# Kernel tuning notes

Hardware: AMD Instinct MI355X
Metric: run time of the kernel (lower is better)

Reference implementation:

```python
import jax, jax.numpy as jnp
import numpy as np

MD = 40                 # max_displacement
K = 2 * MD + 1          # 81 kernel size -> K*K = 6561 displacements


def setup_inputs() -> dict:
    key = jax.random.key(0)
    k1, k2 = jax.random.split(key)
    b, c, h, w = 2, 128, 64, 96
    x1 = jax.random.normal(k1, (b, c, h, w), dtype=jnp.float32)
    x2 = jax.random.normal(k2, (b, c, h, w), dtype=jnp.float32)
    return {"x1": x1, "x2": x2}


def reference(x1, x2):
    b, c, h, w = x1.shape
    # zero-pad x2 by MD on each spatial side (matches F.pad(x2, (pad,)*4))
    x2p = jnp.pad(x2, ((0, 0), (0, 0), (MD, MD), (MD, MD)))

    # Fused sliding-window correlation: scan over the K*K displacements,
    # slicing a (b,c,h,w) window of x2p and reducing over channels.
    # Avoids the (b,c,K^2,h,w) unfold blow-up entirely.
    def step(carry, s):
        dy = s // K
        dx = s % K
        win = jax.lax.dynamic_slice(x2p, (0, 0, dy, dx), (b, c, h, w))
        return carry, jnp.einsum('bchw,bchw->bhw', x1, win)

    _, corr = jax.lax.scan(step, None, jnp.arange(K * K))  # (K*K, b, h, w)
    corr = jnp.transpose(corr, (1, 0, 2, 3))               # (b, K*K, h, w)
    return corr / jnp.sqrt(jnp.float32(c))
```

## Files before the change

kernel.cpp:

```cpp
#include <hip/hip_runtime.h>

#define CH    128
#define HH    64
#define WW    96
#define MD    40
#define KD    81
#define HW    (HH*WW)
#define CHW   (CH*HW)
#define SCALE 0.08838834764831845f
#define LSTR  64
#define CHUNK (WW*LSTR)
#define WS2_USH ((size_t)2*HH*2*CHUNK)
#define NWG   (HH*KD*2)

typedef __attribute__((ext_vector_type(8))) short bf16x8;
typedef __attribute__((ext_vector_type(4))) float f32x4;

__device__ inline unsigned int pack2bf(float lo, float hi) {
    unsigned int a = __float_as_uint(lo), b = __float_as_uint(hi);
    a = (a + 0x7FFFu + ((a >> 16) & 1u)) >> 16;
    b = (b + 0x7FFFu + ((b >> 16) & 1u)) >> 16;
    return a | (b << 16);
}

__global__ __launch_bounds__(256) void prepack(
    const float* __restrict__ x1, const float* __restrict__ x2,
    unsigned short* __restrict__ ws)
{
    const int y = blockIdx.x;
    const int h = blockIdx.y & 1;
    const int t = blockIdx.y >> 1;
    const int b = blockIdx.z;

    const float* src = (t ? x2 : x1)
        + (size_t)b * CHW + (size_t)(h * 64) * HW + (size_t)y * WW;
    unsigned short* dst = ws + (size_t)t * WS2_USH
        + ((size_t)(b * HH + y) * 2 + h) * CHUNK;

    for (int j = threadIdx.x; j < 8 * WW; j += 256) {
        const int cg = j / WW;
        const int x  = j - cg * WW;
        const float* p = src + (size_t)(cg * 8) * HW + x;
        float f[8];
        #pragma unroll
        for (int i = 0; i < 8; ++i) f[i] = p[(size_t)i * HW];
        uint4 w;
        w.x = pack2bf(f[0], f[1]); w.y = pack2bf(f[2], f[3]);
        w.z = pack2bf(f[4], f[5]); w.w = pack2bf(f[6], f[7]);
        *reinterpret_cast<uint4*>(&dst[(size_t)x * LSTR + cg * 8]) = w;
    }
}

__global__ __launch_bounds__(256, 4) void corr_kernel(
    const unsigned short* __restrict__ ws, float* __restrict__ out)
{
    const int wg  = blockIdx.x;
    const int b   = (wg >= HH * KD) ? 1 : 0;
    const int rem = wg - b * (HH * KD);
    const int dy  = rem >> 6;
    const int y   = rem & 63;
    const int tid = threadIdx.x;

    float* outbase = out + ((size_t)b * (KD * KD) + (size_t)dy * KD) * HW
                         + (size_t)y * WW;

    const int y2 = y + dy - MD;
    if (y2 < 0 || y2 >= HH) {
        const float4 z = make_float4(0.f, 0.f, 0.f, 0.f);
        #pragma unroll
        for (int it = 0; it < 8; ++it) {
            const int idx = it * 256 + tid;
            if (idx < KD * (WW / 4)) {
                const int dx = idx / 24;
                const int x4 = idx - dx * 24;
                *reinterpret_cast<float4*>(outbase + (size_t)dx * HW + x4 * 4) = z;
            }
        }
        return;
    }

    __shared__ __align__(16) char smem[KD * WW * 4];
    float* sG = reinterpret_cast<float*>(smem);

    const unsigned short* wsA = ws + ((size_t)(b * HH + y ) * 2) * CHUNK;
    const unsigned short* wsB = ws + WS2_USH + ((size_t)(b * HH + y2) * 2) * CHUNK;

    const int lane = tid & 63;
    const int wave = tid >> 6;
    const int m0   = (wave >> 1) * 48;
    const int n0   = (wave & 1) * 48;
    const int lr   = lane & 15;
    const int q    = lane >> 4;

    f32x4 acc[3][3];
    #pragma unroll
    for (int i = 0; i < 3; ++i)
        #pragma unroll
        for (int j = 0; j < 3; ++j)
            acc[i][j] = (f32x4){0.f, 0.f, 0.f, 0.f};

    #pragma unroll
    for (int h = 0; h < 2; ++h) {
        const unsigned short* pA = wsA + (size_t)h * CHUNK;
        const unsigned short* pB = wsB + (size_t)h * CHUNK;
        #pragma unroll
        for (int kk = 0; kk < 2; ++kk) {
            const int cl = kk * 32 + q * 8;
            bf16x8 af[3], bg[3];
            #pragma unroll
            for (int i = 0; i < 3; ++i)
                af[i] = *reinterpret_cast<const bf16x8*>(&pB[(m0 + 16 * i + lr) * LSTR + cl]);
            #pragma unroll
            for (int j = 0; j < 3; ++j)
                bg[j] = *reinterpret_cast<const bf16x8*>(&pA[(n0 + 16 * j + lr) * LSTR + cl]);
            #pragma unroll
            for (int i = 0; i < 3; ++i)
                #pragma unroll
                for (int j = 0; j < 3; ++j)
                    acc[i][j] = __builtin_amdgcn_mfma_f32_16x16x32_bf16(
                        af[i], bg[j], acc[i][j], 0, 0, 0);
        }
    }

    #pragma unroll
    for (int i = 0; i < 3; ++i) {
        #pragma unroll
        for (int j = 0; j < 3; ++j) {
            const int col  = n0 + 16 * j + lr;
            const int rowb = m0 + 16 * i + q * 4;
            #pragma unroll
            for (int r = 0; r < 4; ++r) {
                const int dxv = (rowb + r) - col + MD;
                if ((unsigned)dxv < (unsigned)KD) {
                    const int w = (dxv * WW + col) ^ (((dxv >> 2) & 1) << 4);
                    sG[w] = acc[i][j][r] * SCALE;
                }
            }
        }
    }
    __syncthreads();

    int dx = tid / 24;
    int x  = 4 * tid - dx * WW;
    #pragma unroll
    for (int it = 0; it < 8; ++it) {
        if (it < 7 || tid < 152) {
            const int baddr = ((dx * WW + x) << 2) ^ (((dx >> 2) & 1) << 6);
            float4 v = *reinterpret_cast<const float4*>(smem + baddr);
            const int x2b = x + dx - MD;
            v.x = ((unsigned)(x2b + 0) < (unsigned)WW) ? v.x : 0.f;
            v.y = ((unsigned)(x2b + 1) < (unsigned)WW) ? v.y : 0.f;
            v.z = ((unsigned)(x2b + 2) < (unsigned)WW) ? v.z : 0.f;
            v.w = ((unsigned)(x2b + 3) < (unsigned)WW) ? v.w : 0.f;
            *reinterpret_cast<float4*>(outbase + (size_t)(dx * HW + x)) = v;
        }
        x += 64; dx += 10;
        if (x >= WW) { x -= WW; ++dx; }
    }
}

extern "C" void kernel_launch(void* const* d_in, const int* in_sizes, int n_in,
                              void* d_out, int out_size, void* d_ws, size_t ws_size,
                              hipStream_t stream) {
    const float* x1 = (const float*)d_in[0];
    const float* x2 = (const float*)d_in[1];
    float* out = (float*)d_out;
    unsigned short* ws = (unsigned short*)d_ws;

    hipLaunchKernelGGL(prepack, dim3(HH, 4, 2), dim3(256), 0, stream, x1, x2, ws);

    hipLaunchKernelGGL(corr_kernel, dim3(NWG), dim3(256), 0, stream, ws, out);
}
```

Before: 374.8 us.

## Make correlation workgroups persistent over dy to reuse x1 fragments in registers

```diff
diff --git a/kernel.cpp b/kernel.cpp
--- a/kernel.cpp
+++ b/kernel.cpp
@@ -8,10 +8,11 @@
 #define HW    (HH*WW)
 #define CHW   (CH*HW)
 #define SCALE 0.08838834764831845f
-#define LSTR  64
+#define LSTR  72
 #define CHUNK (WW*LSTR)
 #define WS2_USH ((size_t)2*HH*2*CHUNK)
-#define NWG   (HH*KD*2)
+#define NCH   16
+#define NWG   (2*HH*NCH)
 
 typedef __attribute__((ext_vector_type(8))) short bf16x8;
 typedef __attribute__((ext_vector_type(4))) float f32x4;
@@ -21,6 +22,12 @@
     a = (a + 0x7FFFu + ((a >> 16) & 1u)) >> 16;
     b = (b + 0x7FFFu + ((b >> 16) & 1u)) >> 16;
     return a | (b << 16);
+}
+
+__device__ __forceinline__ void gload16(const void* g, void* l) {
+    __builtin_amdgcn_global_load_lds(
+        (const __attribute__((address_space(1))) void*)g,
+        (__attribute__((address_space(3))) void*)l, 16, 0, 0);
 }
 
 __global__ __launch_bounds__(256) void prepack(
@@ -55,35 +62,14 @@
     const unsigned short* __restrict__ ws, float* __restrict__ out)
 {
     const int wg  = blockIdx.x;
-    const int b   = (wg >= HH * KD) ? 1 : 0;
-    const int rem = wg - b * (HH * KD);
-    const int dy  = rem >> 6;
-    const int y   = rem & 63;
+    const int y   = wg & 63;
+    const int c   = (wg >> 6) & 15;
+    const int b   = wg >> 10;
     const int tid = threadIdx.x;
 
-    float* outbase = out + ((size_t)b * (KD * KD) + (size_t)dy * KD) * HW
-                         + (size_t)y * WW;
-
-    const int y2 = y + dy - MD;
-    if (y2 < 0 || y2 >= HH) {
-        const float4 z = make_float4(0.f, 0.f, 0.f, 0.f);
-        #pragma unroll
-        for (int it = 0; it < 8; ++it) {
-            const int idx = it * 256 + tid;
-            if (idx < KD * (WW / 4)) {
-                const int dx = idx / 24;
-                const int x4 = idx - dx * 24;
-                *reinterpret_cast<float4*>(outbase + (size_t)dx * HW + x4 * 4) = z;
-            }
-        }
-        return;
-    }
-
-    __shared__ __align__(16) char smem[KD * WW * 4];
-    float* sG = reinterpret_cast<float*>(smem);
-
-    const unsigned short* wsA = ws + ((size_t)(b * HH + y ) * 2) * CHUNK;
-    const unsigned short* wsB = ws + WS2_USH + ((size_t)(b * HH + y2) * 2) * CHUNK;
+    __shared__ __align__(16) char smem[2 * 2 * CHUNK];
+    unsigned short* sX2 = reinterpret_cast<unsigned short*>(smem);
+    unsigned short* sD  = reinterpret_cast<unsigned short*>(smem);
 
     const int lane = tid & 63;
     const int wave = tid >> 6;
@@ -92,70 +78,120 @@
     const int lr   = lane & 15;
     const int q    = lane >> 4;
 
-    f32x4 acc[3][3];
+    const unsigned short* wsA = ws + ((size_t)(b * HH + y) * 2) * CHUNK;
+    bf16x8 xf[2][2][3];
     #pragma unroll
-    for (int i = 0; i < 3; ++i)
-        #pragma unroll
-        for (int j = 0; j < 3; ++j)
-            acc[i][j] = (f32x4){0.f, 0.f, 0.f, 0.f};
-
-    #pragma unroll
-    for (int h = 0; h < 2; ++h) {
-        const unsigned short* pA = wsA + (size_t)h * CHUNK;
-        const unsigned short* pB = wsB + (size_t)h * CHUNK;
-        #pragma unroll
-        for (int kk = 0; kk < 2; ++kk) {
-            const int cl = kk * 32 + q * 8;
-            bf16x8 af[3], bg[3];
-            #pragma unroll
-            for (int i = 0; i < 3; ++i)
-                af[i] = *reinterpret_cast<const bf16x8*>(&pB[(m0 + 16 * i + lr) * LSTR + cl]);
+    for (int h = 0; h < 2; ++h)
+        #pragma unroll
+        for (int kk = 0; kk < 2; ++kk)
             #pragma unroll
             for (int j = 0; j < 3; ++j)
-                bg[j] = *reinterpret_cast<const bf16x8*>(&pA[(n0 + 16 * j + lr) * LSTR + cl]);
-            #pragma unroll
-            for (int i = 0; i < 3; ++i)
+                xf[h][kk][j] = *reinterpret_cast<const bf16x8*>(
+                    &wsA[h * CHUNK + (n0 + 16 * j + lr) * LSTR + kk * 32 + q * 8]);
+
+    const unsigned short* wsB0 = ws + WS2_USH + ((size_t)b * HH * 2) * CHUNK;
+
+    #pragma unroll 1
+    for (int dy = c; dy < KD; dy += NCH) {
+        float* outbase = out + ((size_t)b * (KD * KD) + (size_t)dy * KD) * HW
+                             + (size_t)y * WW;
+        const int y2 = y + dy - MD;
+
+        if (y2 < 0 || y2 >= HH) {
+            const float4 z = make_float4(0.f, 0.f, 0.f, 0.f);
+            #pragma unroll
+            for (int it = 0; it < 8; ++it) {
+                const int idx = it * 256 + tid;
+                if (idx < KD * (WW / 4)) {
+                    const int dx = idx / 24;
+                    const int x4 = idx - dx * 24;
+                    *reinterpret_cast<float4*>(outbase + (size_t)dx * HW + x4 * 4) = z;
+                }
+            }
+            continue;
+        }
+
+        __syncthreads();
+
+        const unsigned short* g2 = wsB0 + (size_t)y2 * 2 * CHUNK;
+        #pragma unroll
+        for (int it = 0; it < 7; ++it) {
+            const int idx = it * 256 + tid;
+            if (idx < 2 * CHUNK / 8)
+                gload16(g2 + (size_t)idx * 8, sX2 + (size_t)idx * 8);
+        }
+        __syncthreads();
+
+        f32x4 acc[3][3];
+        #pragma unroll
+        for (int i = 0; i < 3; ++i)
+            #pragma unroll
+            for (int j = 0; j < 3; ++j)
+                acc[i][j] = (f32x4){0.f, 0.f, 0.f, 0.f};
+
+        #pragma unroll
+        for (int h = 0; h < 2; ++h) {
+            #pragma unroll
+            for (int kk = 0; kk < 2; ++kk) {
+                const int cl = kk * 32 + q * 8;
+                bf16x8 af[3];
                 #pragma unroll
-                for (int j = 0; j < 3; ++j)
-                    acc[i][j] = __builtin_amdgcn_mfma_f32_16x16x32_bf16(
-                        af[i], bg[j], acc[i][j], 0, 0, 0);
-        }
-    }
-
-    #pragma unroll
-    for (int i = 0; i < 3; ++i) {
-        #pragma unroll
-        for (int j = 0; j < 3; ++j) {
-            const int col  = n0 + 16 * j + lr;
-            const int rowb = m0 + 16 * i + q * 4;
-            #pragma unroll
-            for (int r = 0; r < 4; ++r) {
-                const int dxv = (rowb + r) - col + MD;
-                if ((unsigned)dxv < (unsigned)KD) {
-                    const int w = (dxv * WW + col) ^ (((dxv >> 2) & 1) << 4);
-                    sG[w] = acc[i][j][r] * SCALE;
+                for (int i = 0; i < 3; ++i)
+                    af[i] = *reinterpret_cast<const bf16x8*>(
+                        &sX2[h * CHUNK + (m0 + 16 * i + lr) * LSTR + cl]);
+                #pragma unroll
+                for (int i = 0; i < 3; ++i)
+                    #pragma unroll
+                    for (int j = 0; j < 3; ++j)
+                        acc[i][j] = __builtin_amdgcn_mfma_f32_16x16x32_bf16(
+                            af[i], xf[h][kk][j], acc[i][j], 0, 0, 0);
+            }
+        }
+        __syncthreads();
+
+        #pragma unroll
+        for (int i = 0; i < 3; ++i) {
+            #pragma unroll
+            for (int j = 0; j < 3; ++j) {
+                const int col  = n0 + 16 * j + lr;
+                const int rowb = m0 + 16 * i + q * 4;
+                #pragma unroll
+                for (int r = 0; r < 4; ++r) {
+                    const int dxv = (rowb + r) - col + MD;
+                    if ((unsigned)dxv < (unsigned)KD) {
+                        const unsigned int u =
+                            __float_as_uint(acc[i][j][r] * SCALE);
+                        const unsigned short h16 = (unsigned short)
+                            ((u + 0x7FFFu + ((u >> 16) & 1u)) >> 16);
+                        sD[(dxv * WW + col) ^ (((dxv >> 2) & 1) << 3)] = h16;
+                    }
                 }
             }
         }
-    }
-    __syncthreads();
-
-    int dx = tid / 24;
-    int x  = 4 * tid - dx * WW;
-    #pragma unroll
-    for (int it = 0; it < 8; ++it) {
-        if (it < 7 || tid < 152) {
-            const int baddr = ((dx * WW + x) << 2) ^ (((dx >> 2) & 1) << 6);
-            float4 v = *reinterpret_cast<const float4*>(smem + baddr);
-            const int x2b = x + dx - MD;
-            v.x = ((unsigned)(x2b + 0) < (unsigned)WW) ? v.x : 0.f;
-            v.y = ((unsigned)(x2b + 1) < (unsigned)WW) ? v.y : 0.f;
-            v.z = ((unsigned)(x2b + 2) < (unsigned)WW) ? v.z : 0.f;
-            v.w = ((unsigned)(x2b + 3) < (unsigned)WW) ? v.w : 0.f;
-            *reinterpret_cast<float4*>(outbase + (size_t)(dx * HW + x)) = v;
-        }
-        x += 64; dx += 10;
-        if (x >= WW) { x -= WW; ++dx; }
+        __syncthreads();
+
+        int dx = tid / 24;
+        int x  = 4 * (tid - dx * 24);
+        #pragma unroll
+        for (int it = 0; it < 8; ++it) {
+            if (it < 7 || tid < 152) {
+                const int w = (dx * WW + x) ^ (((dx >> 2) & 1) << 3);
+                const uint2 pv = *reinterpret_cast<const uint2*>(&sD[w]);
+                float4 v;
+                v.x = __uint_as_float(pv.x << 16);
+                v.y = __uint_as_float(pv.x & 0xFFFF0000u);
+                v.z = __uint_as_float(pv.y << 16);
+                v.w = __uint_as_float(pv.y & 0xFFFF0000u);
+                const int x2b = x + dx - MD;
+                v.x = ((unsigned)(x2b + 0) < (unsigned)WW) ? v.x : 0.f;
+                v.y = ((unsigned)(x2b + 1) < (unsigned)WW) ? v.y : 0.f;
+                v.z = ((unsigned)(x2b + 2) < (unsigned)WW) ? v.z : 0.f;
+                v.w = ((unsigned)(x2b + 3) < (unsigned)WW) ? v.w : 0.f;
+                *reinterpret_cast<float4*>(outbase + (size_t)(dx * HW + x)) = v;
+            }
+            x += 64; dx += 10;
+            if (x >= WW) { x -= WW; ++dx; }
+        }
     }
 }
 
```

After: 455.7 us. 1.22x slower.
